# Optimization experiments

Hardware: AMD Instinct MI355X
Metric: run time of the kernel (lower is better)

## Reference

```python
import jax, jax.numpy as jnp
import numpy as np

# Code / decoder configuration (regular (3,6) QC-LDPC, rate 1/2)
B, N, M, E, ITERS = 128, 24576, 12288, 73728, 10
CN_DEG = 6          # check-node degree (E = M * CN_DEG, and each VN has degree 3)
CLIP = 20.0         # clip_llr (q_bit == 0 -> clamp with straight-through gradient)
BIG = jnp.float32(1e30)  # acts as +inf for segment-min init


def _quantize(llr):
    """q_bit == 0: clamp to [-CLIP, CLIP] with straight-through estimator."""
    q = jnp.clip(llr, -CLIP, CLIP)
    return jax.lax.stop_gradient(q) + (llr - jax.lax.stop_gradient(llr))


def _decode(llr_in, cn_weight, ch_weight, cn_bias, edge_to_vn, edge_to_cn):
    c2v = jnp.zeros((B, E), jnp.float32)
    sum_llr = jnp.zeros((B, N), jnp.float32)
    dec = llr_in
    loss = jnp.float32(0.0)
    for it in range(ITERS):
        # --- channel weight (sharing[2] == 3: per-iteration scalar) ---
        w_ch = llr_in * ch_weight[it]
        # --- VN update: extrinsic sum at each variable node, gathered per edge ---
        v2c = _quantize(w_ch[:, edge_to_vn] + sum_llr[:, edge_to_vn] - c2v)
        # --- CN update (min-sum): per-CN sign parity + extrinsic min via min1/min2 ---
        a = jnp.abs(v2c)                      # [B, E]
        neg = v2c < 0
        parity = jnp.zeros((B, M), jnp.int32).at[:, edge_to_cn].add(neg.astype(jnp.int32)) % 2
        sign_tot = (1 - 2 * parity).astype(jnp.float32)          # [B, M]
        m1 = jnp.full((B, M), BIG, jnp.float32).at[:, edge_to_cn].min(a)
        is_min = a == m1[:, edge_to_cn]
        cnt = jnp.zeros((B, M), jnp.float32).at[:, edge_to_cn].add(is_min.astype(jnp.float32))
        m2 = jnp.full((B, M), BIG, jnp.float32).at[:, edge_to_cn].min(jnp.where(is_min, BIG, a))
        # edge is the unique minimum of its CN -> use second min; otherwise first min
        ext_min = jnp.where(is_min & (cnt[:, edge_to_cn] == 1.0), m2[:, edge_to_cn], m1[:, edge_to_cn])
        sign_e = 1.0 - 2.0 * neg.astype(jnp.float32)
        c2v_raw = sign_tot[:, edge_to_cn] * sign_e * ext_min
        # --- CN weight (sharing[0] == 3: per-iteration scalar) ---
        c2v_w = c2v_raw * cn_weight[it]
        # --- CN bias (offset): subtract from magnitude, negatives clipped to 0 ---
        mag = jax.nn.relu(jnp.abs(c2v_w) - cn_bias[it])
        c2v = _quantize(jnp.sign(c2v_w) * mag)
        # --- marginal accumulation + decision ---
        sum_llr = jnp.zeros((B, N), jnp.float32).at[:, edge_to_vn].add(c2v)
        dec = llr_in + sum_llr
        # BCE loss assuming all-zero codeword (bit 0 <-> positive LLR), multi-iter
        loss = loss + jnp.mean(jax.nn.softplus(-dec))
    return loss, dec


def setup_inputs() -> dict:
    key = jax.random.key(0)
    # AWGN-like channel LLRs for the all-zero codeword (mostly positive)
    llr_in = 2.0 + 2.0 * jax.random.normal(key, (B, N), dtype=jnp.float32)
    # Structured regular graph: edge e -> CN e // 6, edge e -> VN e % N
    edge_to_vn = jnp.arange(E, dtype=jnp.int32) % N    # each VN has degree 3
    edge_to_cn = jnp.arange(E, dtype=jnp.int32) // CN_DEG  # each CN has degree 6
    return {
        "llr_in": llr_in,
        "cn_weight": jnp.ones((ITERS,), jnp.float32),         # init_cn_weight = 1.0
        "ch_weight": jnp.ones((ITERS,), jnp.float32),         # init_ch_weight = 1.0
        "cn_bias": jnp.full((ITERS,), 0.3, jnp.float32),      # init_cn_bias = 0.3
        "edge_to_vn": edge_to_vn,
        "edge_to_cn": edge_to_cn,
    }


def reference(llr_in, cn_weight, ch_weight, cn_bias, edge_to_vn, edge_to_cn):
    return _decode(llr_in, cn_weight, ch_weight, cn_bias, edge_to_vn, edge_to_cn)
```

## Files before the change

### kernel.cpp

```cpp
#include <hip/hip_runtime.h>
#include <math.h>

#define B_     128
#define N_     24576
#define NCOMP_ 4096
#define ITERS_ 10
#define CLIP_  20.0f
#define NBLOCKS_ ((B_ * NCOMP_) / 256)


__device__ __forceinline__ float clipf(float x) {
    return fminf(fmaxf(x, -CLIP_), CLIP_);
}
__device__ __forceinline__ float clamp0c(float x) {
    return fminf(fmaxf(x, 0.f), CLIP_);
}
__device__ __forceinline__ float fmin3(float a, float b, float c) {
    return fminf(fminf(a, b), c);
}
__device__ __forceinline__ float fmed3(float a, float b, float c) {
    return __builtin_amdgcn_fmed3f(a, b, c);
}
__device__ __forceinline__ float rfl(float x) {
    return __uint_as_float(__builtin_amdgcn_readfirstlane(__float_as_uint(x)));
}

__global__ __launch_bounds__(256, 6) void ldpc_fused_kernel(
    const float* __restrict__ llr_in,
    const float* __restrict__ cn_weight,
    const float* __restrict__ ch_weight,
    const float* __restrict__ cn_bias,
    float* __restrict__ out,
    double* __restrict__ partials)
{
    const int gid = blockIdx.x * 256 + threadIdx.x;
    const int b = gid >> 12;
    const int k = gid & (NCOMP_ - 1);

    float cwv[ITERS_], cnwa[ITERS_], nbias[ITERS_];
    unsigned cnws[ITERS_];
#pragma unroll
    for (int i = 0; i < ITERS_; ++i) {
        float w  = rfl(cn_weight[i]);
        cwv[i]   = rfl(ch_weight[i]);
        cnwa[i]  = fabsf(w);
        cnws[i]  = __float_as_uint(w) & 0x80000000u;
        nbias[i] = -rfl(cn_bias[i]);
    }

    const float2* p2 = (const float2*)(llr_in + b * N_ + 6 * k);
    float2 t0 = p2[0], t1 = p2[1], t2 = p2[2];
    float llr[6] = {t0.x, t0.y, t1.x, t1.y, t2.x, t2.y};

    float c2v[3][6];
    float sum[6];
#pragma unroll
    for (int i = 0; i < 6; ++i) {
        sum[i] = 0.f;
        c2v[0][i] = 0.f; c2v[1][i] = 0.f; c2v[2][i] = 0.f;
    }

    float accMax  = 0.f;
    float prodLog = 1.f;

#pragma unroll
    for (int it = 0; it < ITERS_; ++it) {
        const float cw = cwv[it];

        float u6[6];
#pragma unroll
        for (int i = 0; i < 6; ++i) u6[i] = fmaf(llr[i], cw, sum[i]);

#pragma unroll
        for (int cn = 0; cn < 3; ++cn) {
            float t[6];
            unsigned par = cnws[it];
#pragma unroll
            for (int j = 0; j < 6; ++j) {
                t[j] = clipf(u6[j] - c2v[cn][j]);
                par ^= __float_as_uint(t[j]);
            }
            float minA = fmin3(fabsf(t[0]), fabsf(t[1]), fabsf(t[2]));
            float medA = fmed3(fabsf(t[0]), fabsf(t[1]), fabsf(t[2]));
            float minB = fmin3(fabsf(t[3]), fabsf(t[4]), fabsf(t[5]));
            float medB = fmed3(fabsf(t[3]), fabsf(t[4]), fabsf(t[5]));
            float m1 = fminf(minA, minB);
            float m2 = fmin3(fmaxf(minA, minB), medA, medB);
            float M1p = clamp0c(fmaf(m1, cnwa[it], nbias[it]));
            float M2p = clamp0c(fmaf(m2, cnwa[it], nbias[it]));
#pragma unroll
            for (int j = 0; j < 6; ++j) {
                float ext = (fabsf(t[j]) == m1) ? M2p : M1p;
                unsigned sx = par ^ __float_as_uint(t[j]);
                c2v[cn][j] = __uint_as_float((sx & 0x80000000u)
                                             | __float_as_uint(ext));
            }
        }

#pragma unroll
        for (int i = 0; i < 6; ++i) {
            sum[i] = (c2v[0][i] + c2v[1][i]) + c2v[2][i];
            float dec = llr[i] + sum[i];
            accMax  += fmaxf(-dec, 0.f);
            prodLog *= 1.f + __expf(-fabsf(dec));
        }
    }

    float2* outd = (float2*)(out + 1 + b * N_ + 6 * k);
    outd[0] = make_float2(llr[0] + sum[0], llr[1] + sum[1]);
    outd[1] = make_float2(llr[2] + sum[2], llr[3] + sum[3]);
    outd[2] = make_float2(llr[4] + sum[4], llr[5] + sum[5]);

    float local_loss = accMax + __logf(prodLog);
#pragma unroll
    for (int off = 32; off > 0; off >>= 1)
        local_loss += __shfl_down(local_loss, off);
    __shared__ float wsum[4];
    const int lane = threadIdx.x & 63;
    const int wid  = threadIdx.x >> 6;
    if (lane == 0) wsum[wid] = local_loss;
    __syncthreads();
    if (threadIdx.x == 0) {
        double t = ((double)wsum[0] + (double)wsum[1])
                 + ((double)wsum[2] + (double)wsum[3]);
        partials[blockIdx.x] = t;
    }
}

__global__ __launch_bounds__(256) void ldpc_finalize_kernel(
    const double* __restrict__ partials,
    float* __restrict__ out)
{
    double s = 0.0;
#pragma unroll
    for (int i = 0; i < NBLOCKS_ / 256; ++i)
        s += partials[threadIdx.x + 256 * i];
#pragma unroll
    for (int off = 32; off > 0; off >>= 1)
        s += __shfl_down(s, off);
    __shared__ double wsum[4];
    const int lane = threadIdx.x & 63;
    const int wid  = threadIdx.x >> 6;
    if (lane == 0) wsum[wid] = s;
    __syncthreads();
    if (threadIdx.x == 0) {
        double total = (wsum[0] + wsum[1]) + (wsum[2] + wsum[3]);
        out[0] = (float)(total * (1.0 / ((double)B_ * (double)N_)));
    }
}

extern "C" void kernel_launch(void* const* d_in, const int* in_sizes, int n_in,
                              void* d_out, int out_size, void* d_ws, size_t ws_size,
                              hipStream_t stream) {
    const float* llr_in    = (const float*)d_in[0];
    const float* cn_weight = (const float*)d_in[1];
    const float* ch_weight = (const float*)d_in[2];
    const float* cn_bias   = (const float*)d_in[3];

    float*  out      = (float*)d_out;
    double* partials = (double*)d_ws;

    ldpc_fused_kernel<<<NBLOCKS_, 256, 0, stream>>>(
        llr_in, cn_weight, ch_weight, cn_bias, out, partials);
    ldpc_finalize_kernel<<<1, 256, 0, stream>>>(partials, out);
}
```

Measured before the change: 90.35 us.

## Process two variable-node groups per thread with rolled iteration loop and med3 clamps

Each thread now decodes two independent 6-element groups (12 LLRs) loaded and stored as float4, which halves the thread count and adds instruction-level parallelism between the groups. The iteration loop is no longer unrolled, and the per-iteration weights are read inside it instead of being kept in precomputed register arrays, to reduce code size and register pressure. Clamps use a single v_med3 instead of a min/max pair, and launch bounds drop from 6 to 4 waves per SIMD. The risk is lower occupancy and fewer waves to hide latency, plus a small loop overhead.

New measurement: 104.9 us. 16.1% more time.

```diff
diff --git a/kernel.cpp b/kernel.cpp
--- a/kernel.cpp
+++ b/kernel.cpp
@@ -1,31 +1,27 @@
 #include <hip/hip_runtime.h>
 #include <math.h>
 
-#define B_     128
-#define N_     24576
-#define NCOMP_ 4096
-#define ITERS_ 10
-#define CLIP_  20.0f
-#define NBLOCKS_ ((B_ * NCOMP_) / 256)
+#define B_      128
+#define N_      24576
+#define NPAIR_  2048
+#define ITERS_  10
+#define CLIP_   20.0f
+#define NBLOCKS_ ((B_ * NPAIR_) / 256)
 
 
-__device__ __forceinline__ float clipf(float x) {
-    return fminf(fmaxf(x, -CLIP_), CLIP_);
+__device__ __forceinline__ float fmed3(float a, float b, float c) {
+    return __builtin_amdgcn_fmed3f(a, b, c);
 }
-__device__ __forceinline__ float clamp0c(float x) {
-    return fminf(fmaxf(x, 0.f), CLIP_);
-}
+__device__ __forceinline__ float clipf(float x)   { return fmed3(x, -CLIP_, CLIP_); }
+__device__ __forceinline__ float clamp0c(float x) { return fmed3(x, 0.0f, CLIP_); }
 __device__ __forceinline__ float fmin3(float a, float b, float c) {
     return fminf(fminf(a, b), c);
-}
-__device__ __forceinline__ float fmed3(float a, float b, float c) {
-    return __builtin_amdgcn_fmed3f(a, b, c);
 }
 __device__ __forceinline__ float rfl(float x) {
     return __uint_as_float(__builtin_amdgcn_readfirstlane(__float_as_uint(x)));
 }
 
-__global__ __launch_bounds__(256, 6) void ldpc_fused_kernel(
+__global__ __launch_bounds__(256, 4) void ldpc_fused_kernel(
     const float* __restrict__ llr_in,
     const float* __restrict__ cn_weight,
     const float* __restrict__ ch_weight,
@@ -34,84 +30,92 @@
     double* __restrict__ partials)
 {
     const int gid = blockIdx.x * 256 + threadIdx.x;
-    const int b = gid >> 12;
-    const int k = gid & (NCOMP_ - 1);
+    const int b = gid >> 11;
+    const int p = gid & (NPAIR_ - 1);
 
-    float cwv[ITERS_], cnwa[ITERS_], nbias[ITERS_];
-    unsigned cnws[ITERS_];
+    const float4* p4 = (const float4*)(llr_in + b * N_ + 12 * p);
+    float4 q0 = p4[0], q1 = p4[1], q2 = p4[2];
+    float llr[2][6] = {
+        { q0.x, q0.y, q0.z, q0.w, q1.x, q1.y },
+        { q1.z, q1.w, q2.x, q2.y, q2.z, q2.w }
+    };
+
+    float c2v[2][3][6];
+    float sum[2][6];
 #pragma unroll
-    for (int i = 0; i < ITERS_; ++i) {
-        float w  = rfl(cn_weight[i]);
-        cwv[i]   = rfl(ch_weight[i]);
-        cnwa[i]  = fabsf(w);
-        cnws[i]  = __float_as_uint(w) & 0x80000000u;
-        nbias[i] = -rfl(cn_bias[i]);
-    }
+    for (int g = 0; g < 2; ++g)
+#pragma unroll
+        for (int i = 0; i < 6; ++i) {
+            sum[g][i] = 0.f;
+            c2v[g][0][i] = 0.f; c2v[g][1][i] = 0.f; c2v[g][2][i] = 0.f;
+        }
 
-    const float2* p2 = (const float2*)(llr_in + b * N_ + 6 * k);
-    float2 t0 = p2[0], t1 = p2[1], t2 = p2[2];
-    float llr[6] = {t0.x, t0.y, t1.x, t1.y, t2.x, t2.y};
+    float accMax[2]  = { 0.f, 0.f };
+    float prodLog[2] = { 1.f, 1.f };
 
-    float c2v[3][6];
-    float sum[6];
-#pragma unroll
-    for (int i = 0; i < 6; ++i) {
-        sum[i] = 0.f;
-        c2v[0][i] = 0.f; c2v[1][i] = 0.f; c2v[2][i] = 0.f;
-    }
-
-    float accMax  = 0.f;
-    float prodLog = 1.f;
+#pragma unroll 1
+    for (int it = 0; it < ITERS_; ++it) {
+        const float    cw    = rfl(ch_weight[it]);
+        const float    w     = rfl(cn_weight[it]);
+        const float    cnwa  = fabsf(w);
+        const unsigned cnws  = __float_as_uint(w) & 0x80000000u;
+        const float    nbias = -rfl(cn_bias[it]);
 
 #pragma unroll
-    for (int it = 0; it < ITERS_; ++it) {
-        const float cw = cwv[it];
-
-        float u6[6];
+        for (int g = 0; g < 2; ++g) {
+            float u6[6];
 #pragma unroll
-        for (int i = 0; i < 6; ++i) u6[i] = fmaf(llr[i], cw, sum[i]);
+            for (int i = 0; i < 6; ++i) u6[i] = fmaf(llr[g][i], cw, sum[g][i]);
 
 #pragma unroll
-        for (int cn = 0; cn < 3; ++cn) {
-            float t[6];
-            unsigned par = cnws[it];
+            for (int cn = 0; cn < 3; ++cn) {
+                float t[6];
+                unsigned par = cnws;
 #pragma unroll
-            for (int j = 0; j < 6; ++j) {
-                t[j] = clipf(u6[j] - c2v[cn][j]);
-                par ^= __float_as_uint(t[j]);
+                for (int j = 0; j < 6; ++j) {
+                    t[j] = clipf(u6[j] - c2v[g][cn][j]);
+                    par ^= __float_as_uint(t[j]);
+                }
+                float minA = fmin3(fabsf(t[0]), fabsf(t[1]), fabsf(t[2]));
+                float medA = fmed3(fabsf(t[0]), fabsf(t[1]), fabsf(t[2]));
+                float minB = fmin3(fabsf(t[3]), fabsf(t[4]), fabsf(t[5]));
+                float medB = fmed3(fabsf(t[3]), fabsf(t[4]), fabsf(t[5]));
+                float m1 = fminf(minA, minB);
+                float m2 = fmin3(fmaxf(minA, minB), medA, medB);
+                float M1p = clamp0c(fmaf(m1, cnwa, nbias));
+                float M2p = clamp0c(fmaf(m2, cnwa, nbias));
+#pragma unroll
+                for (int j = 0; j < 6; ++j) {
+                    float ext = (fabsf(t[j]) == m1) ? M2p : M1p;
+                    unsigned sx = par ^ __float_as_uint(t[j]);
+                    c2v[g][cn][j] = __uint_as_float((sx & 0x80000000u)
+                                                    | __float_as_uint(ext));
+                }
             }
-            float minA = fmin3(fabsf(t[0]), fabsf(t[1]), fabsf(t[2]));
-            float medA = fmed3(fabsf(t[0]), fabsf(t[1]), fabsf(t[2]));
-            float minB = fmin3(fabsf(t[3]), fabsf(t[4]), fabsf(t[5]));
-            float medB = fmed3(fabsf(t[3]), fabsf(t[4]), fabsf(t[5]));
-            float m1 = fminf(minA, minB);
-            float m2 = fmin3(fmaxf(minA, minB), medA, medB);
-            float M1p = clamp0c(fmaf(m1, cnwa[it], nbias[it]));
-            float M2p = clamp0c(fmaf(m2, cnwa[it], nbias[it]));
-#pragma unroll
-            for (int j = 0; j < 6; ++j) {
-                float ext = (fabsf(t[j]) == m1) ? M2p : M1p;
-                unsigned sx = par ^ __float_as_uint(t[j]);
-                c2v[cn][j] = __uint_as_float((sx & 0x80000000u)
-                                             | __float_as_uint(ext));
-            }
-        }
 
 #pragma unroll
-        for (int i = 0; i < 6; ++i) {
-            sum[i] = (c2v[0][i] + c2v[1][i]) + c2v[2][i];
-            float dec = llr[i] + sum[i];
-            accMax  += fmaxf(-dec, 0.f);
-            prodLog *= 1.f + __expf(-fabsf(dec));
+            for (int i = 0; i < 6; ++i) {
+                sum[g][i] = (c2v[g][0][i] + c2v[g][1][i]) + c2v[g][2][i];
+                float dec = llr[g][i] + sum[g][i];
+                accMax[g]  += fmaxf(-dec, 0.f);
+                prodLog[g] *= 1.f + __expf(-fabsf(dec));
+            }
         }
     }
 
-    float2* outd = (float2*)(out + 1 + b * N_ + 6 * k);
-    outd[0] = make_float2(llr[0] + sum[0], llr[1] + sum[1]);
-    outd[1] = make_float2(llr[2] + sum[2], llr[3] + sum[3]);
-    outd[2] = make_float2(llr[4] + sum[4], llr[5] + sum[5]);
+    float d[12];
+#pragma unroll
+    for (int g = 0; g < 2; ++g)
+#pragma unroll
+        for (int i = 0; i < 6; ++i) d[6 * g + i] = llr[g][i] + sum[g][i];
 
-    float local_loss = accMax + __logf(prodLog);
+    float4* outd = (float4*)(out + 1 + b * N_ + 12 * p);
+    outd[0] = make_float4(d[0], d[1], d[2],  d[3]);
+    outd[1] = make_float4(d[4], d[5], d[6],  d[7]);
+    outd[2] = make_float4(d[8], d[9], d[10], d[11]);
+
+    float local_loss = (accMax[0] + __logf(prodLog[0]))
+                     + (accMax[1] + __logf(prodLog[1]));
 #pragma unroll
     for (int off = 32; off > 0; off >>= 1)
         local_loss += __shfl_down(local_loss, off);
```

## Move c2v messages to LDS and raise occupancy target to 8 waves

Applied to the files above, without the earlier changes.

Stores the 18 per-thread check-to-variable messages in shared memory (one column per thread, so accesses are conflict-free) instead of registers. The running VN sum is now accumulated while the messages are produced. The launch bound asks for 8 blocks per CU instead of 6, and the clamps use the fmed3 instruction. The aim is to lower VGPR pressure so more waves are resident. In exchange every iteration adds LDS reads and writes, and the 18 KB of LDS per block may itself limit occupancy.

Result: slower. 102.6 us (+13.6%).

```diff
diff --git a/kernel.cpp b/kernel.cpp
--- a/kernel.cpp
+++ b/kernel.cpp
@@ -9,23 +9,19 @@
 #define NBLOCKS_ ((B_ * NCOMP_) / 256)
 
 
-__device__ __forceinline__ float clipf(float x) {
-    return fminf(fmaxf(x, -CLIP_), CLIP_);
+__device__ __forceinline__ float fmed3(float a, float b, float c) {
+    return __builtin_amdgcn_fmed3f(a, b, c);
 }
-__device__ __forceinline__ float clamp0c(float x) {
-    return fminf(fmaxf(x, 0.f), CLIP_);
-}
+__device__ __forceinline__ float clipf(float x)   { return fmed3(x, -CLIP_, CLIP_); }
+__device__ __forceinline__ float clamp0c(float x) { return fmed3(x, 0.0f, CLIP_); }
 __device__ __forceinline__ float fmin3(float a, float b, float c) {
     return fminf(fminf(a, b), c);
-}
-__device__ __forceinline__ float fmed3(float a, float b, float c) {
-    return __builtin_amdgcn_fmed3f(a, b, c);
 }
 __device__ __forceinline__ float rfl(float x) {
     return __uint_as_float(__builtin_amdgcn_readfirstlane(__float_as_uint(x)));
 }
 
-__global__ __launch_bounds__(256, 6) void ldpc_fused_kernel(
+__global__ __launch_bounds__(256, 8) void ldpc_fused_kernel(
     const float* __restrict__ llr_in,
     const float* __restrict__ cn_weight,
     const float* __restrict__ ch_weight,
@@ -33,7 +29,11 @@
     float* __restrict__ out,
     double* __restrict__ partials)
 {
-    const int gid = blockIdx.x * 256 + threadIdx.x;
+    __shared__ float c2v_lds[18][256];
+    __shared__ float wsum[4];
+
+    const int tid = threadIdx.x;
+    const int gid = blockIdx.x * 256 + tid;
     const int b = gid >> 12;
     const int k = gid & (NCOMP_ - 1);
 
@@ -52,13 +52,10 @@
     float2 t0 = p2[0], t1 = p2[1], t2 = p2[2];
     float llr[6] = {t0.x, t0.y, t1.x, t1.y, t2.x, t2.y};
 
-    float c2v[3][6];
-    float sum[6];
 #pragma unroll
-    for (int i = 0; i < 6; ++i) {
-        sum[i] = 0.f;
-        c2v[0][i] = 0.f; c2v[1][i] = 0.f; c2v[2][i] = 0.f;
-    }
+    for (int r = 0; r < 18; ++r) c2v_lds[r][tid] = 0.f;
+
+    float sum[6] = {0.f, 0.f, 0.f, 0.f, 0.f, 0.f};
 
     float accMax  = 0.f;
     float prodLog = 1.f;
@@ -77,7 +74,7 @@
             unsigned par = cnws[it];
 #pragma unroll
             for (int j = 0; j < 6; ++j) {
-                t[j] = clipf(u6[j] - c2v[cn][j]);
+                t[j] = clipf(u6[j] - c2v_lds[cn * 6 + j][tid]);
                 par ^= __float_as_uint(t[j]);
             }
             float minA = fmin3(fabsf(t[0]), fabsf(t[1]), fabsf(t[2]));
@@ -92,14 +89,15 @@
             for (int j = 0; j < 6; ++j) {
                 float ext = (fabsf(t[j]) == m1) ? M2p : M1p;
                 unsigned sx = par ^ __float_as_uint(t[j]);
-                c2v[cn][j] = __uint_as_float((sx & 0x80000000u)
-                                             | __float_as_uint(ext));
+                float val = __uint_as_float((sx & 0x80000000u)
+                                            | __float_as_uint(ext));
+                c2v_lds[cn * 6 + j][tid] = val;
+                sum[j] = (cn == 0) ? val : (sum[j] + val);
             }
         }
 
 #pragma unroll
         for (int i = 0; i < 6; ++i) {
-            sum[i] = (c2v[0][i] + c2v[1][i]) + c2v[2][i];
             float dec = llr[i] + sum[i];
             accMax  += fmaxf(-dec, 0.f);
             prodLog *= 1.f + __expf(-fabsf(dec));
@@ -115,12 +113,11 @@
 #pragma unroll
     for (int off = 32; off > 0; off >>= 1)
         local_loss += __shfl_down(local_loss, off);
-    __shared__ float wsum[4];
-    const int lane = threadIdx.x & 63;
-    const int wid  = threadIdx.x >> 6;
+    const int lane = tid & 63;
+    const int wid  = tid >> 6;
     if (lane == 0) wsum[wid] = local_loss;
     __syncthreads();
-    if (threadIdx.x == 0) {
+    if (tid == 0) {
         double t = ((double)wsum[0] + (double)wsum[1])
                  + ((double)wsum[2] + (double)wsum[3]);
         partials[blockIdx.x] = t;
```
